# Performance work log

Hardware: AMD Instinct MI355X
Metric: run time of the kernel (lower is better)

The kernel has to match this reference:

```python
import jax, jax.numpy as jnp
import numpy as np

B, T, D = 2, 2048, 1024
H, HD = 16, 64          # num_heads, head_dim (D == H*HD)
NM, DMIX, DDEC = 5, 32, 64  # 5 mix streams (r,k,v,w,g); LoRA ranks per source thresholds


def setup_inputs() -> dict:
    key = jax.random.key(0)
    ks = jax.random.split(key, 18)
    n = lambda i, shape, s: jax.random.normal(ks[i], shape, dtype=jnp.float32) * s
    return {
        "hidden_states": n(0, (B, T, D), 1.0),
        "time_maa_x": n(1, (1, 1, D), 0.5),
        "time_maa_r": n(2, (1, 1, D), 0.1),
        "time_maa_k": n(3, (1, 1, D), 0.1),
        "time_maa_v": n(4, (1, 1, D), 0.1),
        "time_maa_w": n(5, (1, 1, D), 0.1),
        "time_maa_g": n(6, (1, 1, D), 0.1),
        "time_maa_w1": n(7, (D, NM * DMIX), 0.01),
        "time_maa_w2": n(8, (NM, DMIX, D), 0.01),
        "time_decay": n(9, (1, 1, D), 0.5) - 2.0,  # decay_speed-like, negative mean
        "time_decay_w1": n(10, (D, DDEC), 0.01),
        "time_decay_w2": n(11, (DDEC, D), 0.01),
        "Wq": n(12, (D, D), 0.02),
        "Wk": n(13, (D, D), 0.02),
        "Wv": n(14, (D, D), 0.02),
        "Wo": n(15, (D, D), 0.02),
        "Wg": n(16, (D, D), 0.02),
        "bg": jnp.full((D,), 1.227, dtype=jnp.float32),  # gate bias init from source
    }


def _forward(hidden_states, time_maa_x, time_maa_r, time_maa_k, time_maa_v,
             time_maa_w, time_maa_g, time_maa_w1, time_maa_w2, time_decay,
             time_decay_w1, time_decay_w2, Wq, Wk, Wv, Wo, Wg, bg):
    x = hidden_states
    Bsz, Tlen, d = x.shape
    # token shift: dxprev = x_{t-1} - x_t (zeros at t=0)
    xprev = jnp.pad(x, ((0, 0), (1, 0), (0, 0)))[:, :Tlen]
    dxprev = xprev - x
    # data-dependent LoRA mixing producing 5 per-stream mix coefficients
    xxx = x + dxprev * time_maa_x
    mix = jnp.tanh(xxx @ time_maa_w1).reshape(Bsz, Tlen, NM, DMIX)
    mix = jnp.einsum('btfl,fld->fbtd', mix, time_maa_w2)  # (5, B, T, D)
    mr, mk, mv, mw, mg = mix
    xr = x + dxprev * (time_maa_r + mr)
    xk = x + dxprev * (time_maa_k + mk)
    xv = x + dxprev * (time_maa_v + mv)
    xw = x + dxprev * (time_maa_w + mw)
    xg = x + dxprev * (time_maa_g + mg)
    # projections -> (B, H, T, HD); num_kv_heads == num_heads so repeat_kv is identity
    q = (xr @ Wq).reshape(Bsz, Tlen, H, HD).transpose(0, 2, 1, 3)
    k = (xk @ Wk).reshape(Bsz, Tlen, H, HD).transpose(0, 2, 1, 3)
    v = (xv @ Wv).reshape(Bsz, Tlen, H, HD).transpose(0, 2, 1, 3)
    decay = time_decay + jnp.tanh(xw @ time_decay_w1) @ time_decay_w2
    g_log = -jnp.exp(decay.reshape(Bsz, Tlen, H, HD).transpose(0, 2, 1, 3))  # (B,H,T,HD), <= 0
    gate = jax.nn.silu(xg @ Wg + bg)
    # bonus term from source: k scaled by (1 - exp(g_log))
    k = k * (1.0 - jnp.exp(g_log))
    q = q * (HD ** -0.5)  # fla scale
    # gated linear attention: S_t = diag(exp(g_t)) S_{t-1} + k_t v_t^T ; o_t = q_t @ S_t
    def step(S, qkvg):
        qt, kt, vt, gt = qkvg                       # (B,H,HD) each
        S = S * jnp.exp(gt)[..., None] + kt[..., None] * vt[..., None, :]
        ot = jnp.einsum('bhk,bhkv->bhv', qt, S)
        return S, ot
    S0 = jnp.zeros((Bsz, H, HD, HD), dtype=jnp.float32)
    seq = (jnp.moveaxis(q, 2, 0), jnp.moveaxis(k, 2, 0),
           jnp.moveaxis(v, 2, 0), jnp.moveaxis(g_log, 2, 0))
    _, o = jax.lax.scan(step, S0, seq)              # (T, B, H, HD)
    o = jnp.moveaxis(o, 0, 1)                       # (B, T, H, HD)
    o = o.reshape(Bsz, Tlen, H * HD)
    return (o * gate) @ Wo


def reference(hidden_states, time_maa_x, time_maa_r, time_maa_k, time_maa_v,
              time_maa_w, time_maa_g, time_maa_w1, time_maa_w2, time_decay,
              time_decay_w1, time_decay_w2, Wq, Wk, Wv, Wo, Wg, bg):
    return _forward(hidden_states, time_maa_x, time_maa_r, time_maa_k, time_maa_v,
                    time_maa_w, time_maa_g, time_maa_w1, time_maa_w2, time_decay,
                    time_decay_w1, time_decay_w2, Wq, Wk, Wv, Wo, Wg, bg)
```

## Files before the change

### kernel.cpp

```cpp
#include <hip/hip_runtime.h>
#include <hip/hip_bf16.h>

typedef __hip_bfloat16 bf16;
typedef __bf16 bf16x8 __attribute__((ext_vector_type(8)));
typedef float f32x4 __attribute__((ext_vector_type(4)));
typedef _Float16 h8 __attribute__((ext_vector_type(8)));

static constexpr size_t MB = 1ull << 20;
static constexpr size_t KB = 1024;

static constexpr size_t OFF_XXXQ = 0;
static constexpr size_t OFF_K    = 8 * MB;
static constexpr size_t OFF_V    = 16 * MB;
static constexpr size_t OFF_W    = 24 * MB;
static constexpr size_t OFF_WQT  = 32 * MB;
static constexpr size_t OFF_WKT  = 34 * MB;
static constexpr size_t OFF_MP   = 36 * MB;
static constexpr size_t OFF_GATE = 32 * MB;
static constexpr size_t OFF_XS0  = 40 * MB;
static constexpr size_t OFF_XS1  = 48 * MB;
static constexpr size_t OFF_SLOC = 40 * MB;
static constexpr size_t OFF_WVT  = 56 * MB;
static constexpr size_t OFF_WGT  = 58 * MB;
static constexpr size_t OFF_WOT  = 60 * MB;
static constexpr size_t OFF_W1T  = 62 * MB;
static constexpr size_t OFF_D    = 62 * MB;
static constexpr size_t OFF_WD1T = 62 * MB + 512 * KB;
static constexpr size_t OFF_WD2T = 62 * MB + 768 * KB;
static constexpr size_t OFF_DECT = 63 * MB;

__device__ __forceinline__ void async_ld16(const void* g, void* l) {
    __builtin_amdgcn_global_load_lds((const __attribute__((address_space(1))) void*)g,
                                     (__attribute__((address_space(3))) void*)l, 16, 0, 0);
}
__device__ __forceinline__ float bf2f(unsigned short u) {
    union { unsigned int i; float f; } x; x.i = ((unsigned int)u) << 16; return x.f;
}

__global__ void transpose_all(const float* __restrict__ Wq, const float* __restrict__ Wk,
                              const float* __restrict__ Wv, const float* __restrict__ Wg,
                              const float* __restrict__ Wo, const float* __restrict__ w1,
                              const float* __restrict__ dw1, const float* __restrict__ dw2,
                              bf16* __restrict__ wqt, bf16* __restrict__ wkt,
                              bf16* __restrict__ wvt, bf16* __restrict__ wgt,
                              bf16* __restrict__ wot, bf16* __restrict__ w1t,
                              bf16* __restrict__ wd1t, bf16* __restrict__ wd2t) {
    __shared__ bf16 tile[32][33];
    int id = blockIdx.x;
    const float* src; bf16* dst; int R, C, Cpad, local;
    if      (id < 1024) { src = Wq;  dst = wqt;  R = 1024; C = 1024; Cpad = 1024; local = id; }
    else if (id < 2048) { src = Wk;  dst = wkt;  R = 1024; C = 1024; Cpad = 1024; local = id - 1024; }
    else if (id < 3072) { src = Wv;  dst = wvt;  R = 1024; C = 1024; Cpad = 1024; local = id - 2048; }
    else if (id < 4096) { src = Wg;  dst = wgt;  R = 1024; C = 1024; Cpad = 1024; local = id - 3072; }
    else if (id < 5120) { src = Wo;  dst = wot;  R = 1024; C = 1024; Cpad = 1024; local = id - 4096; }
    else if (id < 5376) { src = w1;  dst = w1t;  R = 1024; C = 160;  Cpad = 256;  local = id - 5120; }
    else if (id < 5504) { src = dw1; dst = wd1t; R = 1024; C = 64;   Cpad = 128;  local = id - 5376; }
    else                { src = dw2; dst = wd2t; R = 64;   C = 1024; Cpad = 1024; local = id - 5504; }
    int Rb = R >> 5;
    int r0 = (local % Rb) * 32, c0 = (local / Rb) * 32;
    int tx = threadIdx.x, ty = threadIdx.y;
#pragma unroll
    for (int yy = 0; yy < 4; ++yy) {
        int r = r0 + ty + yy * 8, c = c0 + tx;
        float v = (r < R && c < C) ? src[(size_t)r * C + c] : 0.f;
        tile[ty + yy * 8][tx] = __float2bfloat16(v);
    }
    __syncthreads();
#pragma unroll
    for (int yy = 0; yy < 4; ++yy) {
        int c = c0 + ty + yy * 8, r = r0 + tx;
        if (c < Cpad && r < R) dst[(size_t)c * R + r] = tile[tx][ty + yy * 8];
    }
}

__global__ void prep_xxx(const float* __restrict__ x, const float* __restrict__ maa_x,
                         bf16* __restrict__ xxx) {
    int i = blockIdx.x * 256 + threadIdx.x;
    int d = i & 1023;
    int t = (i >> 10) & 2047;
    float xv = x[i];
    float xp = (t > 0) ? x[i - 1024] : 0.f;
    xxx[i] = __float2bfloat16(xv + (xp - xv) * maa_x[d]);
}

template<int EPI>
__global__ __launch_bounds__(256)
void gemm_bt(const bf16* __restrict__ A, int lda,
             const bf16* __restrict__ Bt, int ldb,
             void* __restrict__ Cout, int ldc,
             int K, const float* __restrict__ aux)
{
    __shared__ __align__(16) bf16 As[128 * 32];
    __shared__ __align__(16) bf16 Bs[128 * 32];
    const int m0 = blockIdx.x * 128;
    const int n0 = blockIdx.y * 128;
    const int tid = threadIdx.x;
    const int lane = tid & 63;
    const int w = tid >> 6;
    const int wm = w >> 1, wn = w & 1;
    const int row16 = lane & 15;
    const int quad = lane >> 4;

    f32x4 acc[4][4];
#pragma unroll
    for (int mi = 0; mi < 4; ++mi)
#pragma unroll
        for (int ni = 0; ni < 4; ++ni)
            acc[mi][ni] = (f32x4){0.f, 0.f, 0.f, 0.f};

    for (int k0 = 0; k0 < K; k0 += 32) {
        __syncthreads();
#pragma unroll
        for (int j = 0; j < 2; ++j) {
            int i = j * 256 + w * 64 + lane;
            int ri = i >> 2;
            int ci = (i & 3) * 8;
            async_ld16(A  + (size_t)(m0 + ri) * lda + (k0 + ci), As + (size_t)(j * 256 + w * 64) * 8);
            async_ld16(Bt + (size_t)(n0 + ri) * ldb + (k0 + ci), Bs + (size_t)(j * 256 + w * 64) * 8);
        }
        __syncthreads();
        bf16x8 af[4], bfr[4];
#pragma unroll
        for (int mi = 0; mi < 4; ++mi)
            af[mi] = *(const bf16x8*)(As + ((wm * 64 + mi * 16 + row16) * 32 + quad * 8));
#pragma unroll
        for (int ni = 0; ni < 4; ++ni)
            bfr[ni] = *(const bf16x8*)(Bs + ((wn * 64 + ni * 16 + row16) * 32 + quad * 8));
#pragma unroll
        for (int mi = 0; mi < 4; ++mi)
#pragma unroll
            for (int ni = 0; ni < 4; ++ni)
                acc[mi][ni] = __builtin_amdgcn_mfma_f32_16x16x32_bf16(af[mi], bfr[ni], acc[mi][ni], 0, 0, 0);
    }
#pragma unroll
    for (int mi = 0; mi < 4; ++mi)
#pragma unroll
        for (int ni = 0; ni < 4; ++ni)
#pragma unroll
            for (int r = 0; r < 4; ++r) {
                int gr = m0 + wm * 64 + mi * 16 + quad * 4 + r;
                int gc = n0 + wn * 64 + ni * 16 + row16;
                size_t ci = (size_t)gr * ldc + gc;
                float v = acc[mi][ni][r];
                if (EPI == 1) ((float*)Cout)[ci] = tanhf(v);
                else if (EPI == 2) ((bf16*)Cout)[ci] = __float2bfloat16(tanhf(v));
                else if (EPI == 3) {
                    float t = aux[gc] + v;
                    ((bf16*)Cout)[ci] = __float2bfloat16(expf(t));
                } else {
                    ((float*)Cout)[ci] = v;
                }
            }
}

template<int EPI1>
__global__ __launch_bounds__(256)
void gemm_bt2(const bf16* __restrict__ A0, const bf16* __restrict__ A1, int lda,
              const bf16* __restrict__ B0, const bf16* __restrict__ B1, int ldb,
              bf16* __restrict__ C0, bf16* __restrict__ C1, int ldc,
              int K, const float* __restrict__ aux)
{
    __shared__ __align__(16) bf16 As[128 * 32];
    __shared__ __align__(16) bf16 Bs[128 * 32];
    const int z = blockIdx.z;
    const bf16* A  = z ? A1 : A0;
    const bf16* Bt = z ? B1 : B0;
    bf16* Cout     = z ? C1 : C0;
    const int m0 = blockIdx.x * 128;
    const int n0 = blockIdx.y * 128;
    const int tid = threadIdx.x;
    const int lane = tid & 63;
    const int w = tid >> 6;
    const int wm = w >> 1, wn = w & 1;
    const int row16 = lane & 15;
    const int quad = lane >> 4;

    f32x4 acc[4][4];
#pragma unroll
    for (int mi = 0; mi < 4; ++mi)
#pragma unroll
        for (int ni = 0; ni < 4; ++ni)
            acc[mi][ni] = (f32x4){0.f, 0.f, 0.f, 0.f};

    for (int k0 = 0; k0 < K; k0 += 32) {
        __syncthreads();
#pragma unroll
        for (int j = 0; j < 2; ++j) {
            int i = j * 256 + w * 64 + lane;
            int ri = i >> 2;
            int ci = (i & 3) * 8;
            async_ld16(A  + (size_t)(m0 + ri) * lda + (k0 + ci), As + (size_t)(j * 256 + w * 64) * 8);
            async_ld16(Bt + (size_t)(n0 + ri) * ldb + (k0 + ci), Bs + (size_t)(j * 256 + w * 64) * 8);
        }
        __syncthreads();
        bf16x8 af[4], bfr[4];
#pragma unroll
        for (int mi = 0; mi < 4; ++mi)
            af[mi] = *(const bf16x8*)(As + ((wm * 64 + mi * 16 + row16) * 32 + quad * 8));
#pragma unroll
        for (int ni = 0; ni < 4; ++ni)
            bfr[ni] = *(const bf16x8*)(Bs + ((wn * 64 + ni * 16 + row16) * 32 + quad * 8));
#pragma unroll
        for (int mi = 0; mi < 4; ++mi)
#pragma unroll
            for (int ni = 0; ni < 4; ++ni)
                acc[mi][ni] = __builtin_amdgcn_mfma_f32_16x16x32_bf16(af[mi], bfr[ni], acc[mi][ni], 0, 0, 0);
    }
#pragma unroll
    for (int mi = 0; mi < 4; ++mi)
#pragma unroll
        for (int ni = 0; ni < 4; ++ni)
#pragma unroll
            for (int r = 0; r < 4; ++r) {
                int gr = m0 + wm * 64 + mi * 16 + quad * 4 + r;
                int gc = n0 + wn * 64 + ni * 16 + row16;
                size_t ci = (size_t)gr * ldc + gc;
                float v = acc[mi][ni][r];
                if (z == 0 || EPI1 == 5) Cout[ci] = __float2bfloat16(v);
                else {
                    float zz = v + aux[gc];
                    Cout[ci] = __float2bfloat16(zz / (1.f + expf(-zz)));
                }
            }
}

__global__ __launch_bounds__(256)
void mix_stream(const float* __restrict__ mp, const float* __restrict__ w2,
                const float* __restrict__ x, const float* __restrict__ maa_f,
                int f, bf16* __restrict__ xs)
{
    __shared__ float mps[4][32];
    int dg = blockIdx.x, r0 = blockIdx.y * 4, tid = threadIdx.x;
    int d = dg * 256 + tid;
    if (tid < 128) {
        int rr = tid >> 5, l = tid & 31;
        mps[rr][l] = mp[(size_t)(r0 + rr) * 256 + f * 32 + l];
    }
    __syncthreads();
    float acc[4] = {0.f, 0.f, 0.f, 0.f};
#pragma unroll
    for (int l = 0; l < 32; ++l) {
        float wv = w2[(size_t)(f * 32 + l) * 1024 + d];
#pragma unroll
        for (int rr = 0; rr < 4; ++rr) acc[rr] = fmaf(mps[rr][l], wv, acc[rr]);
    }
    float mf = maa_f[d];
#pragma unroll
    for (int rr = 0; rr < 4; ++rr) {
        int r = r0 + rr, t = r & 2047;
        size_t i = (size_t)r * 1024 + d;
        float xv = x[i];
        float xp = (t > 0) ? x[i - 1024] : 0.f;
        xs[i] = __float2bfloat16(xv + (xp - xv) * (mf + acc[rr]));
    }
}

__global__ __launch_bounds__(256)
void mix_stream2(const float* __restrict__ mp, const float* __restrict__ w2,
                 const float* __restrict__ x,
                 const float* __restrict__ maa_a, const float* __restrict__ maa_b,
                 int fa, int fb, bf16* __restrict__ xsa, bf16* __restrict__ xsb)
{
    __shared__ float mpsa[4][32], mpsb[4][32];
    int dg = blockIdx.x, r0 = blockIdx.y * 4, tid = threadIdx.x;
    int d = dg * 256 + tid;
    if (tid < 128) {
        int rr = tid >> 5, l = tid & 31;
        mpsa[rr][l] = mp[(size_t)(r0 + rr) * 256 + fa * 32 + l];
        mpsb[rr][l] = mp[(size_t)(r0 + rr) * 256 + fb * 32 + l];
    }
    __syncthreads();
    float acca[4] = {0.f, 0.f, 0.f, 0.f}, accb[4] = {0.f, 0.f, 0.f, 0.f};
#pragma unroll
    for (int l = 0; l < 32; ++l) {
        float wa = w2[(size_t)(fa * 32 + l) * 1024 + d];
        float wbv = w2[(size_t)(fb * 32 + l) * 1024 + d];
#pragma unroll
        for (int rr = 0; rr < 4; ++rr) {
            acca[rr] = fmaf(mpsa[rr][l], wa, acca[rr]);
            accb[rr] = fmaf(mpsb[rr][l], wbv, accb[rr]);
        }
    }
    float ma = maa_a[d], mb = maa_b[d];
#pragma unroll
    for (int rr = 0; rr < 4; ++rr) {
        int r = r0 + rr, t = r & 2047;
        size_t i = (size_t)r * 1024 + d;
        float xv = x[i];
        float xp = (t > 0) ? x[i - 1024] : 0.f;
        float dx = xp - xv;
        xsa[i] = __float2bfloat16(xv + dx * (ma + acca[rr]));
        xsb[i] = __float2bfloat16(xv + dx * (mb + accb[rr]));
    }
}

__global__ __launch_bounds__(64)
void chunk_state(const bf16* __restrict__ k, const bf16* __restrict__ v,
                 const bf16* __restrict__ w,
                 _Float16* __restrict__ Sloc, float* __restrict__ D)
{
    int c = blockIdx.x, bh = blockIdx.y;
    int b = bh >> 4, h = bh & 15;
    int lane = threadIdx.x;
    __shared__ __align__(16) float sh[2][64];
    size_t base = (size_t)b * 2048 * 1024 + (size_t)h * 64 + (size_t)c * 32 * 1024;

    float S[64];
#pragma unroll
    for (int i = 0; i < 64; ++i) S[i] = 0.f;
    float Dl = 1.f;

    const unsigned short* kp = (const unsigned short*)k;
    const unsigned short* vp = (const unsigned short*)v;
    const unsigned short* wp = (const unsigned short*)w;
    unsigned short kr[4], vr[4], wr[4];
#pragma unroll
    for (int j = 0; j < 4; ++j) {
        size_t a = base + (size_t)j * 1024 + lane;
        kr[j] = kp[a]; vr[j] = vp[a]; wr[j] = wp[a];
    }
    for (int t = 0; t < 32; ++t) {
        int slot = t & 3, p = t & 1;
        float kl = bf2f(kr[slot]);
        float vl = bf2f(vr[slot]);
        float wl = bf2f(wr[slot]);
        if (t + 4 < 32) {
            size_t a = base + (size_t)(t + 4) * 1024 + lane;
            kr[slot] = kp[a]; vr[slot] = vp[a]; wr[slot] = wp[a];
        }
        float el = __expf(-wl);
        float kb = kl * (1.f - el);
        Dl *= el;
        sh[p][lane] = vl;
        __syncthreads();
        const float4* v4 = (const float4*)sh[p];
#pragma unroll
        for (int vv = 0; vv < 16; ++vv) {
            float4 vx = v4[vv];
            int s = vv * 4;
            S[s + 0] = S[s + 0] * el + kb * vx.x;
            S[s + 1] = S[s + 1] * el + kb * vx.y;
            S[s + 2] = S[s + 2] * el + kb * vx.z;
            S[s + 3] = S[s + 3] * el + kb * vx.w;
        }
    }
    _Float16* So = Sloc + ((size_t)bh * 64 + c) * 4096;
#pragma unroll
    for (int i = 0; i < 64; ++i) So[(size_t)i * 64 + lane] = (_Float16)S[i];
    D[((size_t)bh * 64 + c) * 64 + lane] = Dl;
}

__global__ __launch_bounds__(256)
void chunk_combine(_Float16* __restrict__ Sloc, const float* __restrict__ D)
{
    int bh = blockIdx.x;
    int tid = threadIdx.x;
    int k = tid & 63, v0 = tid >> 6;
    float s[16];
#pragma unroll
    for (int j = 0; j < 16; ++j) s[j] = 0.f;
    for (int c = 0; c < 64; ++c) {
        float Dk = D[((size_t)bh * 64 + c) * 64 + k];
        size_t basei = ((size_t)bh * 64 + c) * 4096 + k;
#pragma unroll
        for (int j = 0; j < 16; ++j) {
            size_t idx = basei + (size_t)(v0 + j * 4) * 64;
            float tmp = (float)Sloc[idx];
            Sloc[idx] = (_Float16)s[j];
            s[j] = s[j] * Dk + tmp;
        }
    }
}

__global__ __launch_bounds__(64)
void chunk_out(const bf16* __restrict__ q, const bf16* __restrict__ k,
               const bf16* __restrict__ v, const bf16* __restrict__ w,
               const bf16* gate, const _Float16* __restrict__ S0buf,
               bf16* ag)
{
    int c = blockIdx.x, bh = blockIdx.y;
    int b = bh >> 4, h = bh & 15;
    int lane = threadIdx.x;
    __shared__ __align__(16) float sh[2][3][64];
    size_t base = (size_t)b * 2048 * 1024 + (size_t)h * 64 + (size_t)c * 32 * 1024;

    float S[64];
    const h8* S0 = (const h8*)(S0buf + ((size_t)bh * 64 + c) * 4096 + (size_t)lane * 64);
#pragma unroll
    for (int i = 0; i < 8; ++i) {
        h8 hv = S0[i];
#pragma unroll
        for (int j = 0; j < 8; ++j) S[i * 8 + j] = (float)hv[j];
    }

    const unsigned short* qp = (const unsigned short*)q;
    const unsigned short* kp = (const unsigned short*)k;
    const unsigned short* vp = (const unsigned short*)v;
    const unsigned short* wp = (const unsigned short*)w;
    const unsigned short* gp = (const unsigned short*)gate;
    unsigned short qr[4], kr[4], vr[4], wr[4], gr[4];
#pragma unroll
    for (int j = 0; j < 4; ++j) {
        size_t a = base + (size_t)j * 1024 + lane;
        qr[j] = qp[a]; kr[j] = kp[a]; vr[j] = vp[a]; wr[j] = wp[a]; gr[j] = gp[a];
    }
    for (int t = 0; t < 32; ++t) {
        int slot = t & 3, p = t & 1;
        float ql = bf2f(qr[slot]) * 0.125f;
        float kl = bf2f(kr[slot]);
        float vl = bf2f(vr[slot]);
        float wl = bf2f(wr[slot]);
        float gl = bf2f(gr[slot]);
        if (t + 4 < 32) {
            size_t a = base + (size_t)(t + 4) * 1024 + lane;
            qr[slot] = qp[a]; kr[slot] = kp[a]; vr[slot] = vp[a];
            wr[slot] = wp[a]; gr[slot] = gp[a];
        }
        float el = __expf(-wl);
        sh[p][0][lane] = ql;
        sh[p][1][lane] = kl * (1.f - el);
        sh[p][2][lane] = el;
        __syncthreads();
        const float4* q4 = (const float4*)sh[p][0];
        const float4* k4 = (const float4*)sh[p][1];
        const float4* e4 = (const float4*)sh[p][2];
        float a0 = 0.f, a1 = 0.f, a2 = 0.f, a3 = 0.f;
#pragma unroll
        for (int kk = 0; kk < 16; ++kk) {
            float4 qq = q4[kk], kx = k4[kk], ee = e4[kk];
            int s = kk * 4;
            S[s + 0] = S[s + 0] * ee.x + kx.x * vl; a0 += qq.x * S[s + 0];
            S[s + 1] = S[s + 1] * ee.y + kx.y * vl; a1 += qq.y * S[s + 1];
            S[s + 2] = S[s + 2] * ee.z + kx.z * vl; a2 += qq.z * S[s + 2];
            S[s + 3] = S[s + 3] * ee.w + kx.w * vl; a3 += qq.w * S[s + 3];
        }
        ag[base + (size_t)t * 1024 + lane] = __float2bfloat16(((a0 + a1) + (a2 + a3)) * gl);
    }
}

extern "C" void kernel_launch(void* const* d_in, const int* in_sizes, int n_in,
                              void* d_out, int out_size, void* d_ws, size_t ws_size,
                              hipStream_t stream) {
    const float* x    = (const float*)d_in[0];
    const float* maax = (const float*)d_in[1];
    const float* maar = (const float*)d_in[2];
    const float* maak = (const float*)d_in[3];
    const float* maav = (const float*)d_in[4];
    const float* maaw = (const float*)d_in[5];
    const float* maag = (const float*)d_in[6];
    const float* w1   = (const float*)d_in[7];
    const float* w2   = (const float*)d_in[8];
    const float* td   = (const float*)d_in[9];
    const float* dw1  = (const float*)d_in[10];
    const float* dw2  = (const float*)d_in[11];
    const float* Wq   = (const float*)d_in[12];
    const float* Wk   = (const float*)d_in[13];
    const float* Wv   = (const float*)d_in[14];
    const float* Wo   = (const float*)d_in[15];
    const float* Wg   = (const float*)d_in[16];
    const float* bg   = (const float*)d_in[17];

    char* ws = (char*)d_ws;
    bf16*  xxx   = (bf16*) (ws + OFF_XXXQ);
    bf16*  qb    = (bf16*) (ws + OFF_XXXQ);
    bf16*  kb    = (bf16*) (ws + OFF_K);
    bf16*  vb    = (bf16*) (ws + OFF_V);
    bf16*  wb    = (bf16*) (ws + OFF_W);
    bf16*  gateb = (bf16*) (ws + OFF_GATE);
    bf16*  wqt   = (bf16*) (ws + OFF_WQT);
    bf16*  wkt   = (bf16*) (ws + OFF_WKT);
    float* mp    = (float*)(ws + OFF_MP);
    bf16*  xs0   = (bf16*) (ws + OFF_XS0);
    bf16*  xs1   = (bf16*) (ws + OFF_XS1);
    bf16*  wvt   = (bf16*) (ws + OFF_WVT);
    bf16*  wgt   = (bf16*) (ws + OFF_WGT);
    bf16*  wot   = (bf16*) (ws + OFF_WOT);
    bf16*  w1t   = (bf16*) (ws + OFF_W1T);
    bf16*  wd1t  = (bf16*) (ws + OFF_WD1T);
    bf16*  wd2t  = (bf16*) (ws + OFF_WD2T);
    bf16*  dect  = (bf16*) (ws + OFF_DECT);
    _Float16* Sloc = (_Float16*)(ws + OFF_SLOC);
    float* Dbuf  = (float*)(ws + OFF_D);

    transpose_all<<<5568, dim3(32, 8), 0, stream>>>(Wq, Wk, Wv, Wg, Wo, w1, dw1, dw2,
                                                    wqt, wkt, wvt, wgt, wot, w1t, wd1t, wd2t);
    prep_xxx<<<16384, 256, 0, stream>>>(x, maax, xxx);

    gemm_bt<1><<<dim3(32, 2), 256, 0, stream>>>(xxx, 1024, w1t, 1024, mp, 256, 1024, nullptr);

    mix_stream<<<dim3(4, 1024), 256, 0, stream>>>(mp, w2, x, maaw, 3, xs0);
    gemm_bt<2><<<dim3(32, 1), 256, 0, stream>>>(xs0, 1024, wd1t, 1024, dect, 128, 1024, nullptr);
    gemm_bt<3><<<dim3(32, 8), 256, 0, stream>>>(dect, 128, wd2t, 64, wb, 1024, 64, td);

    mix_stream2<<<dim3(4, 1024), 256, 0, stream>>>(mp, w2, x, maar, maak, 0, 1, xs0, xs1);
    gemm_bt2<5><<<dim3(32, 8, 2), 256, 0, stream>>>(xs0, xs1, 1024, wqt, wkt, 1024,
                                                    qb, kb, 1024, 1024, nullptr);

    mix_stream2<<<dim3(4, 1024), 256, 0, stream>>>(mp, w2, x, maav, maag, 2, 4, xs0, xs1);
    gemm_bt2<4><<<dim3(32, 8, 2), 256, 0, stream>>>(xs0, xs1, 1024, wvt, wgt, 1024,
                                                    vb, gateb, 1024, 1024, bg);

    chunk_state  <<<dim3(64, 32),  64, 0, stream>>>(kb, vb, wb, Sloc, Dbuf);
    chunk_combine<<<32,           256, 0, stream>>>(Sloc, Dbuf);
    chunk_out    <<<dim3(64, 32),  64, 0, stream>>>(qb, kb, vb, wb, gateb, Sloc, gateb);

    gemm_bt<6><<<dim3(32, 8), 256, 0, stream>>>(gateb, 1024, wot, 1024, (float*)d_out, 1024, 1024, nullptr);

    (void)in_sizes; (void)n_in; (void)out_size; (void)ws_size;
}
```

Measured before the change: 502.2 us.

## Rewrite chunked linear attention as MFMA matmuls with 64-token chunks

The per-chunk state build and intra-chunk output computation move from scalar per-token recurrences to the matrix form of chunked linear attention. Decay is folded into q and k through cumulative products and their reciprocals, and the work runs as bf16/f16 MFMA tile products over 64-token chunks, with a causal-masked P@V term plus a Q@S0 term. This removes the serial per-timestep loop and its per-step syncthreads. In exchange the reciprocal of the cumulative decay can grow large within a chunk, which risks bf16/f16 overflow or precision loss. Separately, prep_xxx is merged into the transpose launch to save one kernel launch.

```diff
diff --git a/kernel.cpp b/kernel.cpp
--- a/kernel.cpp
+++ b/kernel.cpp
@@ -3,8 +3,14 @@
 
 typedef __hip_bfloat16 bf16;
 typedef __bf16 bf16x8 __attribute__((ext_vector_type(8)));
+typedef _Float16 f16x8 __attribute__((ext_vector_type(8)));
 typedef float f32x4 __attribute__((ext_vector_type(4)));
-typedef _Float16 h8 __attribute__((ext_vector_type(8)));
+
+#if __has_builtin(__builtin_amdgcn_rcpf)
+#define RCPF(x) __builtin_amdgcn_rcpf(x)
+#else
+#define RCPF(x) (1.0f / (x))
+#endif
 
 static constexpr size_t MB = 1ull << 20;
 static constexpr size_t KB = 1024;
@@ -36,6 +42,9 @@
 __device__ __forceinline__ float bf2f(unsigned short u) {
     union { unsigned int i; float f; } x; x.i = ((unsigned int)u) << 16; return x.f;
 }
+__device__ __forceinline__ unsigned short f2bu(float x) {
+    union { bf16 b; unsigned short u; } c; c.b = __float2bfloat16(x); return c.u;
+}
 
 __global__ void transpose_all(const float* __restrict__ Wq, const float* __restrict__ Wk,
                               const float* __restrict__ Wv, const float* __restrict__ Wg,
@@ -44,9 +53,21 @@
                               bf16* __restrict__ wqt, bf16* __restrict__ wkt,
                               bf16* __restrict__ wvt, bf16* __restrict__ wgt,
                               bf16* __restrict__ wot, bf16* __restrict__ w1t,
-                              bf16* __restrict__ wd1t, bf16* __restrict__ wd2t) {
+                              bf16* __restrict__ wd1t, bf16* __restrict__ wd2t,
+                              const float* __restrict__ xg, const float* __restrict__ maax,
+                              bf16* __restrict__ xxx) {
     __shared__ bf16 tile[32][33];
     int id = blockIdx.x;
+    if (id >= 5568) {
+        int flat = threadIdx.y * 32 + threadIdx.x;
+        int i = (id - 5568) * 256 + flat;
+        int d = i & 1023;
+        int t = (i >> 10) & 2047;
+        float xv = xg[i];
+        float xp = (t > 0) ? xg[i - 1024] : 0.f;
+        xxx[i] = __float2bfloat16(xv + (xp - xv) * maax[d]);
+        return;
+    }
     const float* src; bf16* dst; int R, C, Cpad, local;
     if      (id < 1024) { src = Wq;  dst = wqt;  R = 1024; C = 1024; Cpad = 1024; local = id; }
     else if (id < 2048) { src = Wk;  dst = wkt;  R = 1024; C = 1024; Cpad = 1024; local = id - 1024; }
@@ -71,16 +92,6 @@
         int c = c0 + ty + yy * 8, r = r0 + tx;
         if (c < Cpad && r < R) dst[(size_t)c * R + r] = tile[tx][ty + yy * 8];
     }
-}
-
-__global__ void prep_xxx(const float* __restrict__ x, const float* __restrict__ maa_x,
-                         bf16* __restrict__ xxx) {
-    int i = blockIdx.x * 256 + threadIdx.x;
-    int d = i & 1023;
-    int t = (i >> 10) & 2047;
-    float xv = x[i];
-    float xp = (t > 0) ? x[i - 1024] : 0.f;
-    xxx[i] = __float2bfloat16(xv + (xp - xv) * maa_x[d]);
 }
 
 template<int EPI>
@@ -294,64 +305,92 @@
     }
 }
 
+
 __global__ __launch_bounds__(64)
-void chunk_state(const bf16* __restrict__ k, const bf16* __restrict__ v,
-                 const bf16* __restrict__ w,
-                 _Float16* __restrict__ Sloc, float* __restrict__ D)
+void chunk_state(const bf16* __restrict__ kG, const bf16* __restrict__ vG,
+                 const bf16* __restrict__ wG,
+                 float* __restrict__ Sloc, float* __restrict__ D)
 {
     int c = blockIdx.x, bh = blockIdx.y;
     int b = bh >> 4, h = bh & 15;
     int lane = threadIdx.x;
-    __shared__ __align__(16) float sh[2][64];
-    size_t base = (size_t)b * 2048 * 1024 + (size_t)h * 64 + (size_t)c * 32 * 1024;
-
-    float S[64];
-#pragma unroll
-    for (int i = 0; i < 64; ++i) S[i] = 0.f;
-    float Dl = 1.f;
-
-    const unsigned short* kp = (const unsigned short*)k;
-    const unsigned short* vp = (const unsigned short*)v;
-    const unsigned short* wp = (const unsigned short*)w;
+    int row16 = lane & 15, quad = lane >> 4;
+    __shared__ __align__(16) char smem[2 * 9216 + 256];
+    bf16* sKiAt = (bf16*)smem;
+    bf16* sVt   = (bf16*)(smem + 9216);
+    float* aLs  = (float*)(smem + 18432);
+    size_t base = (size_t)b * 2048 * 1024 + (size_t)h * 64 + (size_t)c * 64 * 1024;
+
+    const unsigned short* kp = (const unsigned short*)kG;
+    const unsigned short* vp = (const unsigned short*)vG;
+    const unsigned short* wp = (const unsigned short*)wG;
     unsigned short kr[4], vr[4], wr[4];
 #pragma unroll
     for (int j = 0; j < 4; ++j) {
         size_t a = base + (size_t)j * 1024 + lane;
         kr[j] = kp[a]; vr[j] = vp[a]; wr[j] = wp[a];
     }
-    for (int t = 0; t < 32; ++t) {
-        int slot = t & 3, p = t & 1;
+    float A = 1.f;
+    union { unsigned short u[8]; uint4 q; } pk, pv;
+    for (int t = 0; t < 64; ++t) {
+        int slot = t & 3;
         float kl = bf2f(kr[slot]);
         float vl = bf2f(vr[slot]);
         float wl = bf2f(wr[slot]);
-        if (t + 4 < 32) {
+        if (t + 4 < 64) {
             size_t a = base + (size_t)(t + 4) * 1024 + lane;
             kr[slot] = kp[a]; vr[slot] = vp[a]; wr[slot] = wp[a];
         }
         float el = __expf(-wl);
+        A *= el;
         float kb = kl * (1.f - el);
-        Dl *= el;
-        sh[p][lane] = vl;
-        __syncthreads();
-        const float4* v4 = (const float4*)sh[p];
-#pragma unroll
-        for (int vv = 0; vv < 16; ++vv) {
-            float4 vx = v4[vv];
-            int s = vv * 4;
-            S[s + 0] = S[s + 0] * el + kb * vx.x;
-            S[s + 1] = S[s + 1] * el + kb * vx.y;
-            S[s + 2] = S[s + 2] * el + kb * vx.z;
-            S[s + 3] = S[s + 3] * el + kb * vx.w;
+        float invA = RCPF(A);
+        pk.u[t & 7] = f2bu(kb * invA);
+        pv.u[t & 7] = f2bu(vl);
+        if ((t & 7) == 7) {
+            *(uint4*)(sKiAt + lane * 72 + (t - 7)) = pk.q;
+            *(uint4*)(sVt   + lane * 72 + (t - 7)) = pv.q;
         }
     }
-    _Float16* So = Sloc + ((size_t)bh * 64 + c) * 4096;
-#pragma unroll
-    for (int i = 0; i < 64; ++i) So[(size_t)i * 64 + lane] = (_Float16)S[i];
-    D[((size_t)bh * 64 + c) * 64 + lane] = Dl;
+    aLs[lane] = A;
+    D[((size_t)bh * 32 + c) * 64 + lane] = A;
+    __syncthreads();
+
+    f32x4 acc[4][4];
+#pragma unroll
+    for (int mi = 0; mi < 4; ++mi)
+#pragma unroll
+        for (int ni = 0; ni < 4; ++ni) acc[mi][ni] = (f32x4){0.f, 0.f, 0.f, 0.f};
+#pragma unroll
+    for (int kit = 0; kit < 2; ++kit) {
+        bf16x8 af[4], bfr[4];
+#pragma unroll
+        for (int mi = 0; mi < 4; ++mi)
+            af[mi] = *(const bf16x8*)(sVt + (mi * 16 + row16) * 72 + kit * 32 + quad * 8);
+#pragma unroll
+        for (int ni = 0; ni < 4; ++ni)
+            bfr[ni] = *(const bf16x8*)(sKiAt + (ni * 16 + row16) * 72 + kit * 32 + quad * 8);
+#pragma unroll
+        for (int mi = 0; mi < 4; ++mi)
+#pragma unroll
+            for (int ni = 0; ni < 4; ++ni)
+                acc[mi][ni] = __builtin_amdgcn_mfma_f32_16x16x32_bf16(af[mi], bfr[ni], acc[mi][ni], 0, 0, 0);
+    }
+    float* So = Sloc + ((size_t)bh * 32 + c) * 4096;
+#pragma unroll
+    for (int mi = 0; mi < 4; ++mi)
+#pragma unroll
+        for (int ni = 0; ni < 4; ++ni)
+#pragma unroll
+            for (int r = 0; r < 4; ++r) {
+                int rv = mi * 16 + quad * 4 + r;
+                int ck = ni * 16 + row16;
+                So[(size_t)rv * 64 + ck] = acc[mi][ni][r] * aLs[ck];
+            }
 }
 
 __global__ __launch_bounds__(256)
-void chunk_combine(_Float16* __restrict__ Sloc, const float* __restrict__ D)
+void chunk_combine(float* __restrict__ Sloc, const float* __restrict__ D)
 {
     int bh = blockIdx.x;
     int tid = threadIdx.x;
@@ -359,82 +398,160 @@
     float s[16];
 #pragma unroll
     for (int j = 0; j < 16; ++j) s[j] = 0.f;
-    for (int c = 0; c < 64; ++c) {
-        float Dk = D[((size_t)bh * 64 + c) * 64 + k];
-        size_t basei = ((size_t)bh * 64 + c) * 4096 + k;
+    for (int c = 0; c < 32; ++c) {
+        float Dk = D[((size_t)bh * 32 + c) * 64 + k];
+        size_t basei = ((size_t)bh * 32 + c) * 4096 + k;
 #pragma unroll
         for (int j = 0; j < 16; ++j) {
             size_t idx = basei + (size_t)(v0 + j * 4) * 64;
-            float tmp = (float)Sloc[idx];
-            Sloc[idx] = (_Float16)s[j];
+            float tmp = Sloc[idx];
+            Sloc[idx] = s[j];
             s[j] = s[j] * Dk + tmp;
         }
     }
 }
 
 __global__ __launch_bounds__(64)
-void chunk_out(const bf16* __restrict__ q, const bf16* __restrict__ k,
-               const bf16* __restrict__ v, const bf16* __restrict__ w,
-               const bf16* gate, const _Float16* __restrict__ S0buf,
-               bf16* ag)
+void chunk_out(const bf16* __restrict__ qG, const bf16* __restrict__ kG,
+               const bf16* __restrict__ vG, const bf16* __restrict__ wG,
+               const bf16* gate, const float* __restrict__ S0buf, bf16* ag)
 {
     int c = blockIdx.x, bh = blockIdx.y;
     int b = bh >> 4, h = bh & 15;
     int lane = threadIdx.x;
-    __shared__ __align__(16) float sh[2][3][64];
-    size_t base = (size_t)b * 2048 * 1024 + (size_t)h * 64 + (size_t)c * 32 * 1024;
-
-    float S[64];
-    const h8* S0 = (const h8*)(S0buf + ((size_t)bh * 64 + c) * 4096 + (size_t)lane * 64);
-#pragma unroll
-    for (int i = 0; i < 8; ++i) {
-        h8 hv = S0[i];
-#pragma unroll
-        for (int j = 0; j < 8; ++j) S[i * 8 + j] = (float)hv[j];
-    }
-
-    const unsigned short* qp = (const unsigned short*)q;
-    const unsigned short* kp = (const unsigned short*)k;
-    const unsigned short* vp = (const unsigned short*)v;
-    const unsigned short* wp = (const unsigned short*)w;
-    const unsigned short* gp = (const unsigned short*)gate;
-    unsigned short qr[4], kr[4], vr[4], wr[4], gr[4];
+    int row16 = lane & 15, quad = lane >> 4;
+    __shared__ __align__(16) char smem[4 * 9216];
+    bf16*     sQA = (bf16*)smem;
+    bf16*     sKiA = (bf16*)(smem + 9216);
+    _Float16* sP  = (_Float16*)(smem + 9216);
+    _Float16* sVt = (_Float16*)(smem + 18432);
+    bf16*     sS0 = (bf16*)(smem + 27648);
+    float*    Obuf = (float*)smem;
+    size_t base = (size_t)b * 2048 * 1024 + (size_t)h * 64 + (size_t)c * 64 * 1024;
+
+    const float* S0g = S0buf + ((size_t)bh * 32 + c) * 4096;
+#pragma unroll 8
+    for (int i = 0; i < 64; ++i)
+        sS0[i * 72 + lane] = __float2bfloat16(S0g[(size_t)i * 64 + lane]);
+
+    const unsigned short* qp = (const unsigned short*)qG;
+    const unsigned short* kp = (const unsigned short*)kG;
+    const unsigned short* vp = (const unsigned short*)vG;
+    const unsigned short* wp = (const unsigned short*)wG;
+    unsigned short qr[4], kr[4], vr[4], wr[4];
 #pragma unroll
     for (int j = 0; j < 4; ++j) {
         size_t a = base + (size_t)j * 1024 + lane;
-        qr[j] = qp[a]; kr[j] = kp[a]; vr[j] = vp[a]; wr[j] = wp[a]; gr[j] = gp[a];
-    }
-    for (int t = 0; t < 32; ++t) {
-        int slot = t & 3, p = t & 1;
-        float ql = bf2f(qr[slot]) * 0.125f;
+        qr[j] = qp[a]; kr[j] = kp[a]; vr[j] = vp[a]; wr[j] = wp[a];
+    }
+    float A = 1.f;
+    union { _Float16 hp[8]; uint4 q; } pv;
+    for (int t = 0; t < 64; ++t) {
+        int slot = t & 3;
+        float ql = bf2f(qr[slot]);
         float kl = bf2f(kr[slot]);
         float vl = bf2f(vr[slot]);
         float wl = bf2f(wr[slot]);
-        float gl = bf2f(gr[slot]);
-        if (t + 4 < 32) {
+        if (t + 4 < 64) {
             size_t a = base + (size_t)(t + 4) * 1024 + lane;
-            qr[slot] = qp[a]; kr[slot] = kp[a]; vr[slot] = vp[a];
-            wr[slot] = wp[a]; gr[slot] = gp[a];
+            qr[slot] = qp[a]; kr[slot] = kp[a]; vr[slot] = vp[a]; wr[slot] = wp[a];
         }
         float el = __expf(-wl);
-        sh[p][0][lane] = ql;
-        sh[p][1][lane] = kl * (1.f - el);
-        sh[p][2][lane] = el;
-        __syncthreads();
-        const float4* q4 = (const float4*)sh[p][0];
-        const float4* k4 = (const float4*)sh[p][1];
-        const float4* e4 = (const float4*)sh[p][2];
-        float a0 = 0.f, a1 = 0.f, a2 = 0.f, a3 = 0.f;
-#pragma unroll
-        for (int kk = 0; kk < 16; ++kk) {
-            float4 qq = q4[kk], kx = k4[kk], ee = e4[kk];
-            int s = kk * 4;
-            S[s + 0] = S[s + 0] * ee.x + kx.x * vl; a0 += qq.x * S[s + 0];
-            S[s + 1] = S[s + 1] * ee.y + kx.y * vl; a1 += qq.y * S[s + 1];
-            S[s + 2] = S[s + 2] * ee.z + kx.z * vl; a2 += qq.z * S[s + 2];
-            S[s + 3] = S[s + 3] * ee.w + kx.w * vl; a3 += qq.w * S[s + 3];
-        }
-        ag[base + (size_t)t * 1024 + lane] = __float2bfloat16(((a0 + a1) + (a2 + a3)) * gl);
+        A *= el;
+        float kb = kl * (1.f - el);
+        float invA = RCPF(A);
+        sQA[t * 72 + lane]  = __float2bfloat16(ql * 0.125f * A);
+        sKiA[t * 72 + lane] = __float2bfloat16(kb * invA);
+        pv.hp[t & 7] = (_Float16)vl;
+        if ((t & 7) == 7) *(uint4*)(sVt + lane * 72 + (t - 7)) = pv.q;
+    }
+    __syncthreads();
+
+    f32x4 pacc[4][4];
+#pragma unroll
+    for (int mi = 0; mi < 4; ++mi)
+#pragma unroll
+        for (int ni = 0; ni < 4; ++ni) pacc[mi][ni] = (f32x4){0.f, 0.f, 0.f, 0.f};
+#pragma unroll
+    for (int kit = 0; kit < 2; ++kit) {
+        bf16x8 af[4], bfr[4];
+#pragma unroll
+        for (int mi = 0; mi < 4; ++mi)
+            af[mi] = *(const bf16x8*)(sQA + (mi * 16 + row16) * 72 + kit * 32 + quad * 8);
+#pragma unroll
+        for (int ni = 0; ni < 4; ++ni)
+            bfr[ni] = *(const bf16x8*)(sKiA + (ni * 16 + row16) * 72 + kit * 32 + quad * 8);
+#pragma unroll
+        for (int mi = 0; mi < 4; ++mi)
+#pragma unroll
+            for (int ni = 0; ni < 4; ++ni)
+                pacc[mi][ni] = __builtin_amdgcn_mfma_f32_16x16x32_bf16(af[mi], bfr[ni], pacc[mi][ni], 0, 0, 0);
+    }
+    __syncthreads();
+#pragma unroll
+    for (int mi = 0; mi < 4; ++mi)
+#pragma unroll
+        for (int ni = 0; ni < 4; ++ni)
+#pragma unroll
+            for (int r = 0; r < 4; ++r) {
+                int rowt = mi * 16 + quad * 4 + r;
+                int cols = ni * 16 + row16;
+                float pvv = (cols <= rowt) ? pacc[mi][ni][r] : 0.f;
+                sP[rowt * 72 + cols] = (_Float16)pvv;
+            }
+    __syncthreads();
+
+    f32x4 oacc[4][4];
+#pragma unroll
+    for (int mi = 0; mi < 4; ++mi)
+#pragma unroll
+        for (int ni = 0; ni < 4; ++ni) oacc[mi][ni] = (f32x4){0.f, 0.f, 0.f, 0.f};
+#pragma unroll
+    for (int kit = 0; kit < 2; ++kit) {
+        f16x8 af[4], bfr[4];
+#pragma unroll
+        for (int mi = 0; mi < 4; ++mi)
+            af[mi] = *(const f16x8*)(sP + (mi * 16 + row16) * 72 + kit * 32 + quad * 8);
+#pragma unroll
+        for (int ni = 0; ni < 4; ++ni)
+            bfr[ni] = *(const f16x8*)(sVt + (ni * 16 + row16) * 72 + kit * 32 + quad * 8);
+#pragma unroll
+        for (int mi = 0; mi < 4; ++mi)
+#pragma unroll
+            for (int ni = 0; ni < 4; ++ni)
+                oacc[mi][ni] = __builtin_amdgcn_mfma_f32_16x16x32_f16(af[mi], bfr[ni], oacc[mi][ni], 0, 0, 0);
+    }
+#pragma unroll
+    for (int kit = 0; kit < 2; ++kit) {
+        bf16x8 af[4], bfr[4];
+#pragma unroll
+        for (int mi = 0; mi < 4; ++mi)
+            af[mi] = *(const bf16x8*)(sQA + (mi * 16 + row16) * 72 + kit * 32 + quad * 8);
+#pragma unroll
+        for (int ni = 0; ni < 4; ++ni)
+            bfr[ni] = *(const bf16x8*)(sS0 + (ni * 16 + row16) * 72 + kit * 32 + quad * 8);
+#pragma unroll
+        for (int mi = 0; mi < 4; ++mi)
+#pragma unroll
+            for (int ni = 0; ni < 4; ++ni)
+                oacc[mi][ni] = __builtin_amdgcn_mfma_f32_16x16x32_bf16(af[mi], bfr[ni], oacc[mi][ni], 0, 0, 0);
+    }
+    __syncthreads();
+#pragma unroll
+    for (int mi = 0; mi < 4; ++mi)
+#pragma unroll
+        for (int ni = 0; ni < 4; ++ni)
+#pragma unroll
+            for (int r = 0; r < 4; ++r)
+                Obuf[(mi * 16 + quad * 4 + r) * 72 + ni * 16 + row16] = oacc[mi][ni][r];
+    __syncthreads();
+    const unsigned short* gp = (const unsigned short*)gate;
+#pragma unroll 8
+    for (int t = 0; t < 64; ++t) {
+        size_t ad = base + (size_t)t * 1024 + lane;
+        float o = Obuf[t * 72 + lane];
+        float g = bf2f(gp[ad]);
+        ag[ad] = __float2bfloat16(o * g);
     }
 }
 
@@ -479,12 +596,12 @@
     bf16*  wd1t  = (bf16*) (ws + OFF_WD1T);
     bf16*  wd2t  = (bf16*) (ws + OFF_WD2T);
     bf16*  dect  = (bf16*) (ws + OFF_DECT);
-    _Float16* Sloc = (_Float16*)(ws + OFF_SLOC);
+    float* Sloc  = (float*)(ws + OFF_SLOC);
     float* Dbuf  = (float*)(ws + OFF_D);
 
-    transpose_all<<<5568, dim3(32, 8), 0, stream>>>(Wq, Wk, Wv, Wg, Wo, w1, dw1, dw2,
-                                                    wqt, wkt, wvt, wgt, wot, w1t, wd1t, wd2t);
-    prep_xxx<<<16384, 256, 0, stream>>>(x, maax, xxx);
+    transpose_all<<<5568 + 16384, dim3(32, 8), 0, stream>>>(
+        Wq, Wk, Wv, Wg, Wo, w1, dw1, dw2,
+        wqt, wkt, wvt, wgt, wot, w1t, wd1t, wd2t, x, maax, xxx);
 
     gemm_bt<1><<<dim3(32, 2), 256, 0, stream>>>(xxx, 1024, w1t, 1024, mp, 256, 1024, nullptr);
 
@@ -500,9 +617,9 @@
     gemm_bt2<4><<<dim3(32, 8, 2), 256, 0, stream>>>(xs0, xs1, 1024, wvt, wgt, 1024,
                                                     vb, gateb, 1024, 1024, bg);
 
-    chunk_state  <<<dim3(64, 32),  64, 0, stream>>>(kb, vb, wb, Sloc, Dbuf);
+    chunk_state  <<<dim3(32, 32),  64, 0, stream>>>(kb, vb, wb, Sloc, Dbuf);
     chunk_combine<<<32,           256, 0, stream>>>(Sloc, Dbuf);
-    chunk_out    <<<dim3(64, 32),  64, 0, stream>>>(qb, kb, vb, wb, gateb, Sloc, gateb);
+    chunk_out    <<<dim3(32, 32),  64, 0, stream>>>(qb, kb, vb, wb, gateb, Sloc, gateb);
 
     gemm_bt<6><<<dim3(32, 8), 256, 0, stream>>>(gateb, 1024, wot, 1024, (float*)d_out, 1024, 1024, nullptr);
 
```

Result: slower. 517.1 us (+3.0%).
